# Optimization experiments

Hardware: AMD Instinct MI355X
Metric: run time of the kernel (lower is better)

The kernel has to match this reference:

```python
import jax, jax.numpy as jnp
import numpy as np
from jax import lax

NEG = -1e9  # stand-in for -inf that keeps gradients finite
T, V, L = 2048, 32000, 8


def setup_inputs() -> dict:
    key = jax.random.key(0)
    k1, k2, k3 = jax.random.split(key, 3)
    # log piece probabilities (valid distribution in log space)
    log_piece_probs = jax.nn.log_softmax(jax.random.normal(k1, (V,), dtype=jnp.float32))
    # match_idx[t, j] = vocab index of the (unique) piece matching sequence[t:t+j+1], or -1
    match_idx = jax.random.randint(k2, (T, L), 0, V, dtype=jnp.int32)
    keep = jax.random.uniform(k3, (T, L)) < 0.3
    keep = keep.at[:, 0].set(True)  # length-1 (single char) pieces always match -> segmentable
    in_range = (jnp.arange(T)[:, None] + jnp.arange(1, L + 1)[None, :]) <= T
    match_idx = jnp.where(keep & in_range, match_idx, -1)
    return {"log_piece_probs": log_piece_probs, "match_idx": match_idx}


def _forward(log_piece_probs, match_idx):
    T_, L_ = match_idx.shape
    V_ = log_piece_probs.shape[0]
    valid = match_idx >= 0
    # w[t, j] = log p(piece matching at pos t with length j+1), NEG if no match
    w = jnp.where(valid, log_piece_probs[jnp.clip(match_idx, 0)], NEG)  # [T, L]
    # wrev[r, j] = w[r - j, j]: contribution ending at position n = r+1 from length j+1
    wrev = jnp.stack(
        [jnp.pad(w[:, j], (j, 0), constant_values=NEG)[:T_] for j in range(L_)], axis=1
    )  # [T, L]

    # forward pass: alpha[n] = logsumexp_l alpha[n-l] + w[n-l, l-1], rolling buffer of last L alphas
    def astep(buf, wr):
        a = jax.nn.logsumexp(buf[::-1] + wr)  # buf[::-1][j] = alpha[n-1-j]
        return jnp.concatenate([buf[1:], a[None]]), a

    abuf0 = jnp.concatenate([jnp.full((L_ - 1,), NEG, jnp.float32), jnp.zeros((1,), jnp.float32)])
    _, a_rest = lax.scan(astep, abuf0, wrev)
    alpha = jnp.concatenate([jnp.zeros((1,), jnp.float32), a_rest])  # [T+1], alpha[0]=0

    # backward pass: beta[t] = logsumexp_l w[t, l-1] + beta[t+l], rolling buffer of next L betas
    def bstep(buf, wt):
        b = jax.nn.logsumexp(wt + buf)  # buf[j] = beta[t+1+j]
        return jnp.concatenate([b[None], buf[:-1]]), b

    bbuf0 = jnp.concatenate([jnp.zeros((1,), jnp.float32), jnp.full((L_ - 1,), NEG, jnp.float32)])
    _, b_rest = lax.scan(bstep, bbuf0, w, reverse=True)
    beta = jnp.concatenate([b_rest, jnp.zeros((1,), jnp.float32)])  # [T+1], beta[T]=0

    # posterior: P[t, i] = exp(alpha[t] + log p_i + beta[t+len] - alpha[T])
    nxt = jnp.arange(T_)[:, None] + jnp.arange(1, L_ + 1)[None, :]  # [T, L]
    beta_next = beta[jnp.clip(nxt, 0, T_)]
    logP = alpha[:T_, None] + w + beta_next - alpha[T_]
    vals = jnp.where(valid, jnp.exp(logP), 0.0)  # [T, L]
    P = jnp.zeros((T_, V_), jnp.float32).at[
        jnp.arange(T_)[:, None], jnp.clip(match_idx, 0)
    ].add(vals)
    return P


def reference(log_piece_probs, match_idx):
    return _forward(log_piece_probs, match_idx)
```

## Files before the change

kernel.cpp:

```cpp
#include <hip/hip_runtime.h>


#define NEGV -1e9f
#define LOG2E 1.4426950408889634f
constexpr int T = 2048;
constexpr int L = 8;
constexpr int V = 32000;
constexpr int NCH = 64;
constexpr int K = 32;
constexpr int BLK = 512;
constexpr int FILLB = 4096;
constexpr int N4 = T * V / 4;
constexpr int CH4 = N4 / FILLB;
constexpr int CPAD = K * 8 + 4;

__device__ __forceinline__ float hexp2(float x) { return __builtin_amdgcn_exp2f(x); }
__device__ __forceinline__ float hlog2(float x) { return __builtin_amdgcn_logf(x); }

__device__ __forceinline__ float lse8v(float t0, float t1, float t2, float t3,
                                       float t4, float t5, float t6, float t7) {
    float m = fmaxf(fmaxf(fmaxf(t0, t1), fmaxf(t2, t3)),
                    fmaxf(fmaxf(t4, t5), fmaxf(t6, t7)));
    float s = hexp2(t0 - m) + hexp2(t1 - m) + hexp2(t2 - m) + hexp2(t3 - m)
            + hexp2(t4 - m) + hexp2(t5 - m) + hexp2(t6 - m) + hexp2(t7 - m);
    return m + hlog2(s);
}

__global__ __launch_bounds__(BLK) void scan_fill_kernel(
        const float* __restrict__ logp, const int* __restrict__ midx,
        float* __restrict__ out, float* __restrict__ alpha, float* __restrict__ beta) {
    const int tid = threadIdx.x;
    const int bx = blockIdx.x;

    if (bx >= 2) {
        float4 z = make_float4(0.f, 0.f, 0.f, 0.f);
        float4* o4 = (float4*)out;
        const int base4 = (bx - 2) * CH4;
        const int end4 = base4 + CH4;
        for (int i = base4 + tid; i < end4; i += BLK) o4[i] = z;
        return;
    }

    __shared__ __align__(16) float sW[NCH * CPAD];
    __shared__ __align__(16) float sPm[NCH * 64];
    __shared__ float sVst[(NCH + 1) * 8];
    __shared__ float sOut[NCH * 33];

    if (bx == 0) {
        for (int o = tid; o < T * L; o += BLK) {
            int r = o >> 3, j = o & 7, t = r - j;
            float v = NEGV;
            if (t >= 0) { int m = midx[(t << 3) + j]; if (m >= 0) v = logp[m] * LOG2E; }
            sW[(r >> 5) * CPAD + (r & 31) * 8 + j] = v;
        }
    } else {
        for (int o = tid; o < T * L; o += BLK) {
            int s = o >> 3, j = o & 7, t = T - 1 - s;
            int m = midx[(t << 3) + j];
            sW[(s >> 5) * CPAD + (s & 31) * 8 + j] = (m >= 0) ? logp[m] * LOG2E : NEGV;
        }
    }
    __syncthreads();

    {
        const int c = tid >> 3, col = tid & 7;
        float q[8];
#pragma unroll
        for (int i = 0; i < 8; ++i) q[i] = (i == col) ? 0.f : NEGV;
        const float* wc = &sW[c * CPAD];
        float4 c0 = *(const float4*)(wc + 0), c1 = *(const float4*)(wc + 4);
        float4 b0 = *(const float4*)(wc + 8), b1 = *(const float4*)(wc + 12);
        for (int k = 0; k < K; ++k) {
            float4 a0, a1;
            if (k + 2 < K) {
                a0 = *(const float4*)(wc + (k + 2) * 8);
                a1 = *(const float4*)(wc + (k + 2) * 8 + 4);
            }
            float top = lse8v(c0.x + q[0], c0.y + q[1], c0.z + q[2], c0.w + q[3],
                              c1.x + q[4], c1.y + q[5], c1.z + q[6], c1.w + q[7]);
#pragma unroll
            for (int i = 7; i > 0; --i) q[i] = q[i - 1];
            q[0] = top;
            c0 = b0; c1 = b1; b0 = a0; b1 = a1;
        }
#pragma unroll
        for (int i = 0; i < 8; ++i) sPm[c * 64 + i * 8 + col] = q[i];
    }
    __syncthreads();

    if (tid < 8) {
        const int r = tid;
        float v = (r == 0) ? 0.f : NEGV;
        float4 r0 = *(const float4*)&sPm[r * 8];
        float4 r1 = *(const float4*)&sPm[r * 8 + 4];
        for (int cc = 0; cc < NCH; ++cc) {
            sVst[cc * 8 + r] = v;
            float4 n0, n1;
            if (cc + 1 < NCH) {
                n0 = *(const float4*)&sPm[(cc + 1) * 64 + r * 8];
                n1 = *(const float4*)&sPm[(cc + 1) * 64 + r * 8 + 4];
            }
            float vb0 = __shfl(v, 0, 8), vb1 = __shfl(v, 1, 8);
            float vb2 = __shfl(v, 2, 8), vb3 = __shfl(v, 3, 8);
            float vb4 = __shfl(v, 4, 8), vb5 = __shfl(v, 5, 8);
            float vb6 = __shfl(v, 6, 8), vb7 = __shfl(v, 7, 8);
            v = lse8v(r0.x + vb0, r0.y + vb1, r0.z + vb2, r0.w + vb3,
                      r1.x + vb4, r1.y + vb5, r1.z + vb6, r1.w + vb7);
            r0 = n0; r1 = n1;
        }
        sVst[NCH * 8 + r] = v;
    }
    __syncthreads();

    if (tid < NCH) {
        const int cc = tid;
        float ab[8];
#pragma unroll
        for (int i = 0; i < 8; ++i) ab[i] = sVst[cc * 8 + i];
        const float* wc = &sW[cc * CPAD];
        float4 c0 = *(const float4*)(wc + 0), c1 = *(const float4*)(wc + 4);
        float4 b0 = *(const float4*)(wc + 8), b1 = *(const float4*)(wc + 12);
        for (int k = 0; k < K; ++k) {
            float4 a0, a1;
            if (k + 2 < K) {
                a0 = *(const float4*)(wc + (k + 2) * 8);
                a1 = *(const float4*)(wc + (k + 2) * 8 + 4);
            }
            float val = lse8v(c0.x + ab[0], c0.y + ab[1], c0.z + ab[2], c0.w + ab[3],
                              c1.x + ab[4], c1.y + ab[5], c1.z + ab[6], c1.w + ab[7]);
            sOut[cc * 33 + k] = val;
#pragma unroll
            for (int i = 7; i > 0; --i) ab[i] = ab[i - 1];
            ab[0] = val;
            c0 = b0; c1 = b1; b0 = a0; b1 = a1;
        }
    }
    __syncthreads();

    if (bx == 0) {
        for (int o = tid; o < T; o += BLK)
            alpha[o + 1] = sOut[(o >> 5) * 33 + (o & 31)];
        if (tid == 0) alpha[0] = 0.f;
    } else {
        for (int o = tid; o < T; o += BLK) {
            int s = T - 1 - o;
            beta[o] = sOut[(s >> 5) * 33 + (s & 31)];
        }
        if (tid == 0) beta[T] = 0.f;
    }
}

__global__ __launch_bounds__(256) void scatter_kernel(
        const float* __restrict__ logp, const int* __restrict__ midx,
        float* __restrict__ out, const float* __restrict__ alpha,
        const float* __restrict__ beta) {
    int i = blockIdx.x * blockDim.x + threadIdx.x;
    if (i >= T * L) return;
    int m = midx[i];
    if (m < 0) return;
    int t = i >> 3, j = i & 7;
    int nx = t + j + 1;
    if (nx > T) nx = T;
    float lp2 = alpha[t] + logp[m] * LOG2E + beta[nx] - alpha[T];
    atomicAdd(&out[(size_t)t * V + m], hexp2(lp2));
}

extern "C" void kernel_launch(void* const* d_in, const int* in_sizes, int n_in,
                              void* d_out, int out_size, void* d_ws, size_t ws_size,
                              hipStream_t stream) {
    const float* logp = (const float*)d_in[0];
    const int*   midx = (const int*)d_in[1];
    float* out = (float*)d_out;

    float* ws    = (float*)d_ws;
    float* alpha = ws;
    float* beta  = alpha + 2064;

    scan_fill_kernel<<<dim3(2 + FILLB), BLK, 0, stream>>>(logp, midx, out, alpha, beta);
    scatter_kernel<<<dim3((T * L) / 256), 256, 0, stream>>>(logp, midx, out, alpha, beta);
}
```

Measured before the change: 286.2 us.

## Fuse scan, zero-fill and scatter into one cooperative kernel with grid sync

Merges the scan/fill kernel and the scatter kernel into a single cooperative launch of 256 blocks. Blocks 2+ zero-fill larger output chunks, blocks 0-1 run the forward/backward scans, then a grid-wide sync precedes the scatter done by all blocks. This removes the second kernel launch and its gap. The cost is a grid barrier, and the 254 fill blocks now each write a much larger slice, which may reduce bandwidth parallelism.

```diff
diff --git a/kernel.cpp b/kernel.cpp
--- a/kernel.cpp
+++ b/kernel.cpp
@@ -1,5 +1,8 @@
 #include <hip/hip_runtime.h>
+#include <hip/hip_cooperative_groups.h>
 
+
+namespace cg = cooperative_groups;
 
 #define NEGV -1e9f
 #define LOG2E 1.4426950408889634f
@@ -9,9 +12,9 @@
 constexpr int NCH = 64;
 constexpr int K = 32;
 constexpr int BLK = 512;
-constexpr int FILLB = 4096;
+constexpr int GRID = 256;
 constexpr int N4 = T * V / 4;
-constexpr int CH4 = N4 / FILLB;
+constexpr int CH4 = (N4 + GRID - 3) / (GRID - 2);
 constexpr int CPAD = K * 8 + 4;
 
 __device__ __forceinline__ float hexp2(float x) { return __builtin_amdgcn_exp2f(x); }
@@ -26,143 +29,142 @@
     return m + hlog2(s);
 }
 
-__global__ __launch_bounds__(BLK) void scan_fill_kernel(
+__global__ __launch_bounds__(BLK) void fused_kernel(
         const float* __restrict__ logp, const int* __restrict__ midx,
         float* __restrict__ out, float* __restrict__ alpha, float* __restrict__ beta) {
     const int tid = threadIdx.x;
     const int bx = blockIdx.x;
-
-    if (bx >= 2) {
-        float4 z = make_float4(0.f, 0.f, 0.f, 0.f);
-        float4* o4 = (float4*)out;
-        const int base4 = (bx - 2) * CH4;
-        const int end4 = base4 + CH4;
-        for (int i = base4 + tid; i < end4; i += BLK) o4[i] = z;
-        return;
-    }
 
     __shared__ __align__(16) float sW[NCH * CPAD];
     __shared__ __align__(16) float sPm[NCH * 64];
     __shared__ float sVst[(NCH + 1) * 8];
     __shared__ float sOut[NCH * 33];
 
-    if (bx == 0) {
-        for (int o = tid; o < T * L; o += BLK) {
-            int r = o >> 3, j = o & 7, t = r - j;
-            float v = NEGV;
-            if (t >= 0) { int m = midx[(t << 3) + j]; if (m >= 0) v = logp[m] * LOG2E; }
-            sW[(r >> 5) * CPAD + (r & 31) * 8 + j] = v;
+    if (bx >= 2) {
+        float4 z = make_float4(0.f, 0.f, 0.f, 0.f);
+        float4* o4 = (float4*)out;
+        const int base4 = (bx - 2) * CH4;
+        int end4 = base4 + CH4; if (end4 > N4) end4 = N4;
+        for (int i = base4 + tid; i < end4; i += BLK) o4[i] = z;
+    } else {
+        if (bx == 0) {
+            for (int o = tid; o < T * L; o += BLK) {
+                int r = o >> 3, j = o & 7, t = r - j;
+                float v = NEGV;
+                if (t >= 0) { int m = midx[(t << 3) + j]; if (m >= 0) v = logp[m] * LOG2E; }
+                sW[(r >> 5) * CPAD + (r & 31) * 8 + j] = v;
+            }
+        } else {
+            for (int o = tid; o < T * L; o += BLK) {
+                int s = o >> 3, j = o & 7, t = T - 1 - s;
+                int m = midx[(t << 3) + j];
+                sW[(s >> 5) * CPAD + (s & 31) * 8 + j] = (m >= 0) ? logp[m] * LOG2E : NEGV;
+            }
         }
-    } else {
-        for (int o = tid; o < T * L; o += BLK) {
-            int s = o >> 3, j = o & 7, t = T - 1 - s;
-            int m = midx[(t << 3) + j];
-            sW[(s >> 5) * CPAD + (s & 31) * 8 + j] = (m >= 0) ? logp[m] * LOG2E : NEGV;
+        __syncthreads();
+
+        {
+            const int c = tid >> 3, col = tid & 7;
+            float q[8];
+#pragma unroll
+            for (int i = 0; i < 8; ++i) q[i] = (i == col) ? 0.f : NEGV;
+            const float* wc = &sW[c * CPAD];
+            float4 c0 = *(const float4*)(wc + 0), c1 = *(const float4*)(wc + 4);
+            float4 b0 = *(const float4*)(wc + 8), b1 = *(const float4*)(wc + 12);
+            for (int k = 0; k < K; ++k) {
+                float4 a0, a1;
+                if (k + 2 < K) {
+                    a0 = *(const float4*)(wc + (k + 2) * 8);
+                    a1 = *(const float4*)(wc + (k + 2) * 8 + 4);
+                }
+                float top = lse8v(c0.x + q[0], c0.y + q[1], c0.z + q[2], c0.w + q[3],
+                                  c1.x + q[4], c1.y + q[5], c1.z + q[6], c1.w + q[7]);
+#pragma unroll
+                for (int i = 7; i > 0; --i) q[i] = q[i - 1];
+                q[0] = top;
+                c0 = b0; c1 = b1; b0 = a0; b1 = a1;
+            }
+#pragma unroll
+            for (int i = 0; i < 8; ++i) sPm[c * 64 + i * 8 + col] = q[i];
+        }
+        __syncthreads();
+
+        if (tid < 8) {
+            const int r = tid;
+            float v = (r == 0) ? 0.f : NEGV;
+            float4 r0 = *(const float4*)&sPm[r * 8];
+            float4 r1 = *(const float4*)&sPm[r * 8 + 4];
+            for (int cc = 0; cc < NCH; ++cc) {
+                sVst[cc * 8 + r] = v;
+                float4 n0, n1;
+                if (cc + 1 < NCH) {
+                    n0 = *(const float4*)&sPm[(cc + 1) * 64 + r * 8];
+                    n1 = *(const float4*)&sPm[(cc + 1) * 64 + r * 8 + 4];
+                }
+                float vb0 = __shfl(v, 0, 8), vb1 = __shfl(v, 1, 8);
+                float vb2 = __shfl(v, 2, 8), vb3 = __shfl(v, 3, 8);
+                float vb4 = __shfl(v, 4, 8), vb5 = __shfl(v, 5, 8);
+                float vb6 = __shfl(v, 6, 8), vb7 = __shfl(v, 7, 8);
+                v = lse8v(r0.x + vb0, r0.y + vb1, r0.z + vb2, r0.w + vb3,
+                          r1.x + vb4, r1.y + vb5, r1.z + vb6, r1.w + vb7);
+                r0 = n0; r1 = n1;
+            }
+            sVst[NCH * 8 + r] = v;
+        }
+        __syncthreads();
+
+        if (tid < NCH) {
+            const int cc = tid;
+            float ab[8];
+#pragma unroll
+            for (int i = 0; i < 8; ++i) ab[i] = sVst[cc * 8 + i];
+            const float* wc = &sW[cc * CPAD];
+            float4 c0 = *(const float4*)(wc + 0), c1 = *(const float4*)(wc + 4);
+            float4 b0 = *(const float4*)(wc + 8), b1 = *(const float4*)(wc + 12);
+            for (int k = 0; k < K; ++k) {
+                float4 a0, a1;
+                if (k + 2 < K) {
+                    a0 = *(const float4*)(wc + (k + 2) * 8);
+                    a1 = *(const float4*)(wc + (k + 2) * 8 + 4);
+                }
+                float val = lse8v(c0.x + ab[0], c0.y + ab[1], c0.z + ab[2], c0.w + ab[3],
+                                  c1.x + ab[4], c1.y + ab[5], c1.z + ab[6], c1.w + ab[7]);
+                sOut[cc * 33 + k] = val;
+#pragma unroll
+                for (int i = 7; i > 0; --i) ab[i] = ab[i - 1];
+                ab[0] = val;
+                c0 = b0; c1 = b1; b0 = a0; b1 = a1;
+            }
+        }
+        __syncthreads();
+
+        if (bx == 0) {
+            for (int o = tid; o < T; o += BLK)
+                alpha[o + 1] = sOut[(o >> 5) * 33 + (o & 31)];
+            if (tid == 0) alpha[0] = 0.f;
+        } else {
+            for (int o = tid; o < T; o += BLK) {
+                int s = T - 1 - o;
+                beta[o] = sOut[(s >> 5) * 33 + (s & 31)];
+            }
+            if (tid == 0) beta[T] = 0.f;
         }
     }
-    __syncthreads();
 
-    {
-        const int c = tid >> 3, col = tid & 7;
-        float q[8];
-#pragma unroll
-        for (int i = 0; i < 8; ++i) q[i] = (i == col) ? 0.f : NEGV;
-        const float* wc = &sW[c * CPAD];
-        float4 c0 = *(const float4*)(wc + 0), c1 = *(const float4*)(wc + 4);
-        float4 b0 = *(const float4*)(wc + 8), b1 = *(const float4*)(wc + 12);
-        for (int k = 0; k < K; ++k) {
-            float4 a0, a1;
-            if (k + 2 < K) {
-                a0 = *(const float4*)(wc + (k + 2) * 8);
-                a1 = *(const float4*)(wc + (k + 2) * 8 + 4);
-            }
-            float top = lse8v(c0.x + q[0], c0.y + q[1], c0.z + q[2], c0.w + q[3],
-                              c1.x + q[4], c1.y + q[5], c1.z + q[6], c1.w + q[7]);
-#pragma unroll
-            for (int i = 7; i > 0; --i) q[i] = q[i - 1];
-            q[0] = top;
-            c0 = b0; c1 = b1; b0 = a0; b1 = a1;
-        }
-#pragma unroll
-        for (int i = 0; i < 8; ++i) sPm[c * 64 + i * 8 + col] = q[i];
-    }
-    __syncthreads();
+    __threadfence();
+    cg::this_grid().sync();
 
-    if (tid < 8) {
-        const int r = tid;
-        float v = (r == 0) ? 0.f : NEGV;
-        float4 r0 = *(const float4*)&sPm[r * 8];
-        float4 r1 = *(const float4*)&sPm[r * 8 + 4];
-        for (int cc = 0; cc < NCH; ++cc) {
-            sVst[cc * 8 + r] = v;
-            float4 n0, n1;
-            if (cc + 1 < NCH) {
-                n0 = *(const float4*)&sPm[(cc + 1) * 64 + r * 8];
-                n1 = *(const float4*)&sPm[(cc + 1) * 64 + r * 8 + 4];
-            }
-            float vb0 = __shfl(v, 0, 8), vb1 = __shfl(v, 1, 8);
-            float vb2 = __shfl(v, 2, 8), vb3 = __shfl(v, 3, 8);
-            float vb4 = __shfl(v, 4, 8), vb5 = __shfl(v, 5, 8);
-            float vb6 = __shfl(v, 6, 8), vb7 = __shfl(v, 7, 8);
-            v = lse8v(r0.x + vb0, r0.y + vb1, r0.z + vb2, r0.w + vb3,
-                      r1.x + vb4, r1.y + vb5, r1.z + vb6, r1.w + vb7);
-            r0 = n0; r1 = n1;
-        }
-        sVst[NCH * 8 + r] = v;
-    }
-    __syncthreads();
-
-    if (tid < NCH) {
-        const int cc = tid;
-        float ab[8];
-#pragma unroll
-        for (int i = 0; i < 8; ++i) ab[i] = sVst[cc * 8 + i];
-        const float* wc = &sW[cc * CPAD];
-        float4 c0 = *(const float4*)(wc + 0), c1 = *(const float4*)(wc + 4);
-        float4 b0 = *(const float4*)(wc + 8), b1 = *(const float4*)(wc + 12);
-        for (int k = 0; k < K; ++k) {
-            float4 a0, a1;
-            if (k + 2 < K) {
-                a0 = *(const float4*)(wc + (k + 2) * 8);
-                a1 = *(const float4*)(wc + (k + 2) * 8 + 4);
-            }
-            float val = lse8v(c0.x + ab[0], c0.y + ab[1], c0.z + ab[2], c0.w + ab[3],
-                              c1.x + ab[4], c1.y + ab[5], c1.z + ab[6], c1.w + ab[7]);
-            sOut[cc * 33 + k] = val;
-#pragma unroll
-            for (int i = 7; i > 0; --i) ab[i] = ab[i - 1];
-            ab[0] = val;
-            c0 = b0; c1 = b1; b0 = a0; b1 = a1;
+    int i = bx * BLK + tid;
+    if (i < T * L) {
+        int m = midx[i];
+        if (m >= 0) {
+            int t = i >> 3, j = i & 7;
+            int nx = t + j + 1;
+            if (nx > T) nx = T;
+            float lp2 = alpha[t] + logp[m] * LOG2E + beta[nx] - alpha[T];
+            atomicAdd(&out[(size_t)t * V + m], hexp2(lp2));
         }
     }
-    __syncthreads();
-
-    if (bx == 0) {
-        for (int o = tid; o < T; o += BLK)
-            alpha[o + 1] = sOut[(o >> 5) * 33 + (o & 31)];
-        if (tid == 0) alpha[0] = 0.f;
-    } else {
-        for (int o = tid; o < T; o += BLK) {
-            int s = T - 1 - o;
-            beta[o] = sOut[(s >> 5) * 33 + (s & 31)];
-        }
-        if (tid == 0) beta[T] = 0.f;
-    }
-}
-
-__global__ __launch_bounds__(256) void scatter_kernel(
-        const float* __restrict__ logp, const int* __restrict__ midx,
-        float* __restrict__ out, const float* __restrict__ alpha,
-        const float* __restrict__ beta) {
-    int i = blockIdx.x * blockDim.x + threadIdx.x;
-    if (i >= T * L) return;
-    int m = midx[i];
-    if (m < 0) return;
-    int t = i >> 3, j = i & 7;
-    int nx = t + j + 1;
-    if (nx > T) nx = T;
-    float lp2 = alpha[t] + logp[m] * LOG2E + beta[nx] - alpha[T];
-    atomicAdd(&out[(size_t)t * V + m], hexp2(lp2));
 }
 
 extern "C" void kernel_launch(void* const* d_in, const int* in_sizes, int n_in,
@@ -176,6 +178,7 @@
     float* alpha = ws;
     float* beta  = alpha + 2064;
 
-    scan_fill_kernel<<<dim3(2 + FILLB), BLK, 0, stream>>>(logp, midx, out, alpha, beta);
-    scatter_kernel<<<dim3((T * L) / 256), 256, 0, stream>>>(logp, midx, out, alpha, beta);
+    void* args[] = {(void*)&logp, (void*)&midx, (void*)&out, (void*)&alpha, (void*)&beta};
+    hipLaunchCooperativeKernel((const void*)fused_kernel, dim3(GRID), dim3(BLK),
+                               args, 0, stream);
 }
```

Result: slower. 388.2 us (+35.6%).
